# Performance work log

Hardware: AMD Instinct MI355X
Metric: run time of the kernel (lower is better)

## Reference

```python
import jax, jax.numpy as jnp
import numpy as np

DIM = 1024
HEADS = 16
HDIM = DIM // HEADS
HIDDEN = 4 * DIM
SCALE = HDIM ** -0.5


def layernorm(x, g, b, eps=1e-5):
    mu = jnp.mean(x, axis=-1, keepdims=True)
    var = jnp.var(x, axis=-1, keepdims=True)
    return (x - mu) * jax.lax.rsqrt(var + eps) * g + b


def setup_inputs() -> dict:
    key = jax.random.key(0)
    ks = jax.random.split(key, 8)
    s = 0.02
    return {
        "x": jax.random.normal(ks[0], (4, 1024, DIM), dtype=jnp.float32),
        "ln1_g": jnp.ones((DIM,), jnp.float32),
        "ln1_b": jnp.zeros((DIM,), jnp.float32),
        "ln2_g": jnp.ones((DIM,), jnp.float32),
        "ln2_b": jnp.zeros((DIM,), jnp.float32),
        "qkv_w": jax.random.normal(ks[1], (DIM, 3 * DIM), jnp.float32) * s,
        "qkv_b": jnp.zeros((3 * DIM,), jnp.float32),
        "proj_w": jax.random.normal(ks[2], (DIM, DIM), jnp.float32) * s,
        "proj_b": jnp.zeros((DIM,), jnp.float32),
        "fc1_w": jax.random.normal(ks[3], (DIM, HIDDEN), jnp.float32) * s,
        "fc1_b": jnp.zeros((HIDDEN,), jnp.float32),
        "fc2_w": jax.random.normal(ks[4], (HIDDEN, DIM), jnp.float32) * s,
        "fc2_b": jnp.zeros((DIM,), jnp.float32),
    }


def reference(x, ln1_g, ln1_b, ln2_g, ln2_b, qkv_w, qkv_b, proj_w, proj_b,
              fc1_w, fc1_b, fc2_w, fc2_b):
    B, N, C = x.shape
    # --- attention branch ---
    h = layernorm(x, ln1_g, ln1_b)
    qkv = h @ qkv_w + qkv_b                       # [B,N,3C]
    qkv = qkv.reshape(B, N, 3, HEADS, HDIM)
    q, k, v = jnp.moveaxis(qkv, 2, 0)             # each [B,N,H,Dh]
    q = jnp.swapaxes(q, 1, 2)                      # [B,H,N,Dh]
    k = jnp.swapaxes(k, 1, 2)
    v = jnp.swapaxes(v, 1, 2)
    attn = jnp.einsum('bhqd,bhkd->bhqk', q, k) * SCALE
    attn = jax.nn.softmax(attn, axis=-1)
    o = jnp.einsum('bhqk,bhkd->bhqd', attn, v)     # [B,H,N,Dh]
    o = jnp.swapaxes(o, 1, 2).reshape(B, N, C)
    x = x + (o @ proj_w + proj_b)
    # --- MLP branch ---
    h = layernorm(x, ln2_g, ln2_b)
    h = jax.nn.gelu(h @ fc1_w + fc1_b, approximate=False)
    x = x + (h @ fc2_w + fc2_b)
    return x
```

## Files before the change

kernel.cpp:

```cpp
#include <hip/hip_runtime.h>
#include <math.h>

#define DIM    1024
#define HEADS  16
#define HDIM   64
#define HIDDEN 4096
#define BATCH  4
#define SEQ    1024
#define ROWS   (BATCH * SEQ)

typedef short s16x8 __attribute__((ext_vector_type(8)));
typedef float f32x4 __attribute__((ext_vector_type(4)));

__device__ __forceinline__ float blo(unsigned int u) {
    union { unsigned int i; float f; } x; x.i = u << 16; return x.f;
}
__device__ __forceinline__ float bhi(unsigned int u) {
    union { unsigned int i; float f; } x; x.i = u & 0xffff0000u; return x.f;
}
__device__ __forceinline__ unsigned short f2b(float f) {
    union { float f; unsigned int i; } x; x.f = f;
    unsigned int r = x.i + 0x7fffu + ((x.i >> 16) & 1u);
    return (unsigned short)(r >> 16);
}

__device__ __forceinline__ float gelu_f(float x) {
    float z  = fabsf(x) * 0.70710678118f;
    float t  = __builtin_amdgcn_rcpf(__builtin_fmaf(0.3275911f, z, 1.0f));
    float p  = ((((1.061405429f * t - 1.453152027f) * t + 1.421413741f) * t
                 - 0.284496736f) * t + 0.254829592f) * t;
    float e  = exp2f(-0.72134752f * x * x);
    float w  = 0.5f * p * e;
    float phi = (x >= 0.0f) ? (1.0f - w) : w;
    return x * phi;
}

__device__ __forceinline__ size_t tidx(int row, int k, int Kdim) {
    return ((size_t)(row >> 4) * (Kdim >> 5) + (k >> 5)) * 512
         + (size_t)(((k & 31) >> 3) * 128 + (row & 15) * 8 + (k & 7));
}

__device__ __forceinline__ void gload_lds16(const void* g, void* l) {
    __builtin_amdgcn_global_load_lds(
        (const __attribute__((address_space(1))) unsigned int*)g,
        (__attribute__((address_space(3))) unsigned int*)l, 16, 0, 0);
}

__global__ __launch_bounds__(256) void prep_kernel(const float* __restrict__ x,
                                                   const float* __restrict__ g,
                                                   const float* __restrict__ b,
                                                   unsigned short* __restrict__ lnout,
                                                   const float* __restrict__ qkv_w,
                                                   unsigned short* __restrict__ wT_qkv,
                                                   const float* __restrict__ proj_w,
                                                   unsigned short* __restrict__ wT_proj,
                                                   const float* __restrict__ fc1_w,
                                                   unsigned short* __restrict__ wT_fc1,
                                                   const float* __restrict__ fc2_w,
                                                   unsigned short* __restrict__ wT_fc2) {
    __shared__ float red1[256], red2[256];
    __shared__ unsigned short T[64][68];
    const int bid = blockIdx.x;
    const int t = threadIdx.x;

    if (bid < ROWS) {
        int row = bid;
        const float* xr = x + (size_t)row * DIM;
        float4 v = *((const float4*)(xr + t * 4));
        float s  = v.x + v.y + v.z + v.w;
        float ss = v.x * v.x + v.y * v.y + v.z * v.z + v.w * v.w;
        red1[t] = s; red2[t] = ss;
        __syncthreads();
        for (int off = 128; off > 0; off >>= 1) {
            if (t < off) { red1[t] += red1[t + off]; red2[t] += red2[t + off]; }
            __syncthreads();
        }
        float mu   = red1[0] * (1.0f / DIM);
        float var  = red2[0] * (1.0f / DIM) - mu * mu;
        float rstd = rsqrtf(var + 1e-5f);
        float4 gv = *((const float4*)(g + t * 4));
        float4 bv = *((const float4*)(b + t * 4));
        ushort4 o;
        o.x = f2b((v.x - mu) * rstd * gv.x + bv.x);
        o.y = f2b((v.y - mu) * rstd * gv.y + bv.y);
        o.z = f2b((v.z - mu) * rstd * gv.z + bv.z);
        o.w = f2b((v.w - mu) * rstd * gv.w + bv.w);
        *((ushort4*)(lnout + tidx(row, t * 4, DIM))) = o;
    } else {
        int tt = bid - ROWS;
        const float* W; unsigned short* Wt; int K, N, bx, by;
        if (tt < 768) {
            W = qkv_w; Wt = wT_qkv; K = DIM; N = 3 * DIM; bx = tt % 48; by = tt / 48;
        } else if (tt < 768 + 256) {
            tt -= 768;
            W = proj_w; Wt = wT_proj; K = DIM; N = DIM; bx = tt % 16; by = tt / 16;
        } else if (tt < 768 + 256 + 1024) {
            tt -= 768 + 256;
            W = fc1_w; Wt = wT_fc1; K = DIM; N = HIDDEN; bx = tt % 64; by = tt / 64;
        } else {
            tt -= 768 + 256 + 1024;
            W = fc2_w; Wt = wT_fc2; K = HIDDEN; N = DIM; bx = tt % 16; by = tt / 16;
        }
        int n0 = bx * 64, k0 = by * 64;
        int cr = t >> 4;
        int cc = (t & 15) * 4;
        #pragma unroll
        for (int r = 0; r < 4; ++r) {
            int kk = cr + 16 * r;
            float4 v = *((const float4*)(W + (size_t)(k0 + kk) * N + n0 + cc));
            T[cc + 0][kk] = f2b(v.x);
            T[cc + 1][kk] = f2b(v.y);
            T[cc + 2][kk] = f2b(v.z);
            T[cc + 3][kk] = f2b(v.w);
        }
        __syncthreads();
        {
            int nn = t >> 2;
            int kg = (t & 3) * 16;
            #pragma unroll
            for (int p = 0; p < 2; ++p) {
                int k8 = kg + p * 8;
                ushort4 lo = *((ushort4*)&T[nn][k8]);
                ushort4 hi = *((ushort4*)&T[nn][k8 + 4]);
                unsigned short* dst = Wt + tidx(n0 + nn, k0 + k8, K);
                *((ushort4*)dst)       = lo;
                *((ushort4*)(dst + 4)) = hi;
            }
        }
    }
}

__global__ __launch_bounds__(256) void reduce_ln(const unsigned short* __restrict__ p0,
                                                 const unsigned short* __restrict__ p1,
                                                 const float* __restrict__ x,
                                                 const float* __restrict__ bias,
                                                 const float* __restrict__ g,
                                                 const float* __restrict__ b,
                                                 float* __restrict__ xout,
                                                 unsigned short* __restrict__ lnout) {
    int row = blockIdx.x;
    int t = threadIdx.x;
    size_t i = (size_t)row * DIM + t * 4;
    float4 xv = *((const float4*)(x + i));
    float4 bi = *((const float4*)(bias + t * 4));
    uint2 w0 = *((const uint2*)(p0 + i));
    uint2 w1 = *((const uint2*)(p1 + i));
    float4 v;
    v.x = xv.x + bi.x + blo(w0.x) + blo(w1.x);
    v.y = xv.y + bi.y + bhi(w0.x) + bhi(w1.x);
    v.z = xv.z + bi.z + blo(w0.y) + blo(w1.y);
    v.w = xv.w + bi.w + bhi(w0.y) + bhi(w1.y);
    *((float4*)(xout + i)) = v;

    float s  = v.x + v.y + v.z + v.w;
    float ss = v.x * v.x + v.y * v.y + v.z * v.z + v.w * v.w;
    __shared__ float red1[256], red2[256];
    red1[t] = s; red2[t] = ss;
    __syncthreads();
    for (int off = 128; off > 0; off >>= 1) {
        if (t < off) { red1[t] += red1[t + off]; red2[t] += red2[t + off]; }
        __syncthreads();
    }
    float mu   = red1[0] * (1.0f / DIM);
    float var  = red2[0] * (1.0f / DIM) - mu * mu;
    float rstd = rsqrtf(var + 1e-5f);
    float4 gv = *((const float4*)(g + t * 4));
    float4 bv = *((const float4*)(b + t * 4));
    ushort4 o;
    o.x = f2b((v.x - mu) * rstd * gv.x + bv.x);
    o.y = f2b((v.y - mu) * rstd * gv.y + bv.y);
    o.z = f2b((v.z - mu) * rstd * gv.z + bv.z);
    o.w = f2b((v.w - mu) * rstd * gv.w + bv.w);
    *((ushort4*)(lnout + tidx(row, t * 4, DIM))) = o;
}

__global__ __launch_bounds__(256, 4) void mfma_gemm(const unsigned short* __restrict__ A,
                                                 const unsigned short* __restrict__ Bt,
                                                 const float* __restrict__ bias,
                                                 void* __restrict__ Cout,
                                                 unsigned short* __restrict__ vt,
                                                 unsigned short* __restrict__ p0,
                                                 unsigned short* __restrict__ p1,
                                                 unsigned short* __restrict__ p2,
                                                 unsigned short* __restrict__ p3,
                                                 int M, int N, int K, int Ksplit, int fuse) {
    __shared__ __align__(16) short Asm[8192];
    __shared__ __align__(16) short Bsm[8192];

    const int tid  = threadIdx.x;
    const int lane = tid & 63;
    const int wave = tid >> 6;
    const int wy = wave >> 1, wx = wave & 1;
    const int lr = lane & 15;
    const int lq = lane >> 4;

    int m_t, n_t;
    {
        const int mt = gridDim.x, ntl = gridDim.y, G = 8;
        if (ntl > G) {
            int lin = blockIdx.y * mt + blockIdx.x;
            int gsz = mt * G;
            int grp = lin / gsz;
            int rem = lin - grp * gsz;
            m_t = rem % mt;
            n_t = grp * G + rem / mt;
        } else { m_t = blockIdx.x; n_t = blockIdx.y; }
    }
    const int m0 = m_t * 128, n0 = n_t * 128;
    const int kbase = blockIdx.z * Ksplit;
    const int kch = K >> 5;

    f32x4 acc[4][4];
    #pragma unroll
    for (int i = 0; i < 4; ++i)
        #pragma unroll
        for (int j = 0; j < 4; ++j)
            acc[i][j] = (f32x4){0.f, 0.f, 0.f, 0.f};

    const unsigned short* ag[4]; const unsigned short* bg[4];
    short* al[4]; short* bl[4];
    #pragma unroll
    for (int j = 0; j < 4; ++j) {
        int cid = wave * 4 + j;
        int mb  = cid >> 1;
        int kc  = cid & 1;
        ag[j] = A  + ((size_t)((m0 >> 4) + mb) * kch + (kbase >> 5) + kc) * 512 + lane * 8;
        bg[j] = Bt + ((size_t)((n0 >> 4) + mb) * kch + (kbase >> 5) + kc) * 512 + lane * 8;
        al[j] = &Asm[cid * 512];
        bl[j] = &Bsm[cid * 512];
    }

    for (int k0 = 0; k0 < Ksplit; k0 += 64) {
        #pragma unroll
        for (int j = 0; j < 4; ++j) {
            gload_lds16(ag[j], al[j]);
            gload_lds16(bg[j], bl[j]);
            ag[j] += 1024; bg[j] += 1024;
        }
        __syncthreads();
        #pragma unroll
        for (int kc = 0; kc < 2; ++kc) {
            s16x8 af[4], bf[4];
            #pragma unroll
            for (int i = 0; i < 4; ++i)
                af[i] = *((const s16x8*)&Asm[((wy * 4 + i) * 2 + kc) * 512 + lane * 8]);
            #pragma unroll
            for (int j = 0; j < 4; ++j)
                bf[j] = *((const s16x8*)&Bsm[((wx * 4 + j) * 2 + kc) * 512 + lane * 8]);
            #pragma unroll
            for (int i = 0; i < 4; ++i)
                #pragma unroll
                for (int j = 0; j < 4; ++j)
                    acc[i][j] = __builtin_amdgcn_mfma_f32_16x16x32_bf16(af[i], bf[j], acc[i][j], 0, 0, 0);
        }
        __syncthreads();
    }

    short* Wl = (wave < 2 ? Asm : Bsm) + (wave & 1) * 4096;

    if (fuse == 0 && vt && (n0 + wx * 64) >= 2 * DIM) {
        #pragma unroll
        for (int j = 0; j < 4; ++j) {
            int col = n0 + wx * 64 + j * 16 + lr;
            float bi = bias[col];
            #pragma unroll
            for (int i = 0; i < 4; ++i) {
                int row0 = m0 + wy * 64 + i * 16 + lq * 4;
                #pragma unroll
                for (int r = 0; r < 4; ++r) {
                    float val = acc[i][j][r] + bi;
                    int row = row0 + r;
                    int b_ = row >> 10, tok = row & 1023;
                    int hd = col - 2 * DIM, h_ = hd >> 6, d = hd & 63;
                    size_t o = (size_t)(b_ * 16 + h_) * 65536
                             + ((size_t)(d >> 4) * 32 + (tok >> 5)) * 512
                             + ((tok & 31) >> 3) * 128 + (d & 15) * 8 + (tok & 7);
                    vt[o] = f2b(val);
                }
            }
        }
    } else if (fuse == 3) {
        #pragma unroll
        for (int j = 0; j < 4; ++j) {
            #pragma unroll
            for (int i = 0; i < 4; ++i) {
                #pragma unroll
                for (int r = 0; r < 4; ++r) {
                    int rowL = i * 16 + lq * 4 + r;
                    int colL = (j * 16 + lr) ^ ((rowL & 7) << 3);
                    Wl[rowL * 64 + colL] = (short)f2b(acc[i][j][r]);
                }
            }
        }
        int z = blockIdx.z;
        unsigned short* P = (z == 0) ? p0 : (z == 1) ? p1 : (z == 2) ? p2 : p3;
        unsigned short* Prow = P + (size_t)(m0 + wy * 64 + lane) * N + n0 + wx * 64;
        #pragma unroll
        for (int c = 0; c < 8; ++c) {
            int colr = (c * 8) ^ ((lane & 7) << 3);
            s16x8 v = *((const s16x8*)&Wl[lane * 64 + colr]);
            *((s16x8*)&Prow[c * 8]) = v;
        }
    } else {
        #pragma unroll
        for (int j = 0; j < 4; ++j) {
            float bi = bias[n0 + wx * 64 + j * 16 + lr];
            #pragma unroll
            for (int i = 0; i < 4; ++i) {
                #pragma unroll
                for (int r = 0; r < 4; ++r) {
                    float val = acc[i][j][r] + bi;
                    if (fuse == 1) val = gelu_f(val);
                    int colL = (j & 1) * 16 + lr;
                    int hi = colL >> 3;
                    int pos = hi * 128 + (lq * 4 + r) * 8 + (lr & 7);
                    pos ^= ((pos >> 7) & 3) << 3;
                    Wl[(i * 2 + (j >> 1)) * 512 + pos] = (short)f2b(val);
                }
            }
        }
        const size_t rc0 = (size_t)((m0 + wy * 64) >> 4);
        const size_t cc0 = (size_t)((n0 + wx * 64) >> 5);
        const size_t nch = (size_t)(N >> 5);
        #pragma unroll
        for (int c = 0; c < 8; ++c) {
            int raddr = lane * 8;
            raddr ^= ((raddr >> 7) & 3) << 3;
            s16x8 v = *((const s16x8*)&Wl[c * 512 + raddr]);
            size_t chunk = (rc0 + (c >> 1)) * nch + cc0 + (c & 1);
            *((s16x8*)&((unsigned short*)Cout)[chunk * 512 + lane * 8]) = v;
        }
    }
}

__global__ __launch_bounds__(256) void reduce_kernel(const unsigned short* __restrict__ p0,
                                                     const unsigned short* __restrict__ p1,
                                                     const unsigned short* __restrict__ p2,
                                                     const unsigned short* __restrict__ p3,
                                                     int S,
                                                     const float* __restrict__ x,
                                                     const float* __restrict__ bias,
                                                     float* __restrict__ out) {
    int i = (blockIdx.x * 256 + threadIdx.x) * 8;
    int col = i & (DIM - 1);
    float4 b0 = *((const float4*)(bias + col));
    float4 b1 = *((const float4*)(bias + col + 4));
    float4 x0 = *((const float4*)(x + i));
    float4 x1 = *((const float4*)(x + i + 4));
    float a[8] = {x0.x + b0.x, x0.y + b0.y, x0.z + b0.z, x0.w + b0.w,
                  x1.x + b1.x, x1.y + b1.y, x1.z + b1.z, x1.w + b1.w};
    const unsigned short* ps[4] = {p0, p1, p2, p3};
    for (int s = 0; s < S; ++s) {
        uint4 w = *((const uint4*)(ps[s] + i));
        a[0] += blo(w.x); a[1] += bhi(w.x);
        a[2] += blo(w.y); a[3] += bhi(w.y);
        a[4] += blo(w.z); a[5] += bhi(w.z);
        a[6] += blo(w.w); a[7] += bhi(w.w);
    }
    *((float4*)(out + i))     = make_float4(a[0], a[1], a[2], a[3]);
    *((float4*)(out + i + 4)) = make_float4(a[4], a[5], a[6], a[7]);
}

__global__ __launch_bounds__(256) void fattn_mfma(const unsigned short* __restrict__ qkv,
                                                  const unsigned short* __restrict__ Vt,
                                                  unsigned short* __restrict__ out) {
    __shared__ __align__(16) short Qs[4096];
    __shared__ __align__(16) short Ks[4096];
    __shared__ __align__(16) short Vs[4096];
    __shared__ __align__(16) short Ps[64 * 72];
    __shared__ __align__(16) short OnesB[512];

    const int tid = threadIdx.x, lane = tid & 63, wave = tid >> 6;
    const int lr = lane & 15, lq = lane >> 4;
    const int L = blockIdx.x;
    const int idx = L >> 3;
    const int qt = idx & 15;
    const int bh = (L & 7) + 8 * (idx >> 4);
    const int b = bh >> 4, h = bh & 15;
    const int q0 = qt * 64;

    {
        s16x8 z = (s16x8){0,0,0,0,0,0,0,0};
        if (lr == 0) { z[0] = (short)0x3F80; z[1] = (short)0x3F80;
                       z[2] = (short)0x3F80; z[3] = (short)0x3F80;
                       z[4] = (short)0x3F80; z[5] = (short)0x3F80;
                       z[6] = (short)0x3F80; z[7] = (short)0x3F80; }
        if (wave == 0) *((s16x8*)&OnesB[lane * 8]) = z;
    }

    #pragma unroll
    for (int j = 0; j < 2; ++j) {
        int cid = wave * 2 + j;
        const unsigned short* g = qkv + ((size_t)(((b * SEQ + q0) >> 4) + (cid >> 1)) * 96
                                         + 2 * h + (cid & 1)) * 512 + lane * 8;
        gload_lds16(g, &Qs[cid * 512]);
    }

    const unsigned short* kg_[2]; const unsigned short* vg_[2];
    short *kl_[2], *vl_[2];
    #pragma unroll
    for (int j = 0; j < 2; ++j) {
        int cid = wave * 2 + j;
        kg_[j] = qkv + ((size_t)(((b * SEQ) >> 4) + (cid >> 1)) * 96
                        + 32 + 2 * h + (cid & 1)) * 512 + lane * 8;
        vg_[j] = Vt + (size_t)bh * 65536
                 + ((size_t)(cid >> 1) * 32 + (cid & 1)) * 512 + lane * 8;
        kl_[j] = &Ks[cid * 512];
        vl_[j] = &Vs[cid * 512];
    }

    f32x4 osum[5];
    #pragma unroll
    for (int d = 0; d < 5; ++d)
        osum[d] = (f32x4){0.f, 0.f, 0.f, 0.f};

    const float c = 0.125f * 1.44269504f;

    for (int k0 = 0; k0 < SEQ; k0 += 64) {
        #pragma unroll
        for (int j = 0; j < 2; ++j) {
            gload_lds16(kg_[j], kl_[j]);
            gload_lds16(vg_[j], vl_[j]);
            kg_[j] += 4 * 96 * 512;
            vg_[j] += 1024;
        }
        __syncthreads();

        f32x4 s[4];
        #pragma unroll
        for (int jb = 0; jb < 4; ++jb)
            s[jb] = (f32x4){0.f, 0.f, 0.f, 0.f};
        __builtin_amdgcn_s_setprio(1);
        #pragma unroll
        for (int kc = 0; kc < 2; ++kc) {
            s16x8 aq = *((const s16x8*)&Qs[(wave * 2 + kc) * 512 + lane * 8]);
            #pragma unroll
            for (int jb = 0; jb < 4; ++jb) {
                s16x8 bk = *((const s16x8*)&Ks[(jb * 2 + kc) * 512 + lane * 8]);
                s[jb] = __builtin_amdgcn_mfma_f32_16x16x32_bf16(aq, bk, s[jb], 0, 0, 0);
            }
        }
        __builtin_amdgcn_s_setprio(0);

        #pragma unroll
        for (int r = 0; r < 4; ++r) {
            int prow = wave * 16 + lq * 4 + r;
            #pragma unroll
            for (int jb = 0; jb < 4; ++jb)
                Ps[prow * 72 + jb * 16 + lr] = (short)f2b(exp2f(s[jb][r] * c));
        }

        __builtin_amdgcn_s_setprio(1);
        #pragma unroll
        for (int kc = 0; kc < 2; ++kc) {
            s16x8 ap = *((const s16x8*)&Ps[(wave * 16 + lr) * 72 + kc * 32 + lq * 8]);
            #pragma unroll
            for (int db = 0; db < 4; ++db) {
                s16x8 bv = *((const s16x8*)&Vs[(db * 2 + kc) * 512 + lane * 8]);
                osum[db] = __builtin_amdgcn_mfma_f32_16x16x32_bf16(ap, bv, osum[db], 0, 0, 0);
            }
            s16x8 bo = *((const s16x8*)&OnesB[lane * 8]);
            osum[4] = __builtin_amdgcn_mfma_f32_16x16x32_bf16(ap, bo, osum[4], 0, 0, 0);
        }
        __builtin_amdgcn_s_setprio(0);
        __syncthreads();
    }

    {
        int qrow = q0 + wave * 16 + lq * 4;
        #pragma unroll
        for (int r = 0; r < 4; ++r) {
            float lsum = __shfl(osum[4][r], lane & 48, 64);
            float inv = 1.0f / lsum;
            int row = b * SEQ + qrow + r;
            #pragma unroll
            for (int db = 0; db < 4; ++db)
                out[tidx(row, h * 64 + db * 16 + lr, DIM)] = f2b(osum[db][r] * inv);
        }
    }
}

extern "C" void kernel_launch(void* const* d_in, const int* in_sizes, int n_in,
                              void* d_out, int out_size, void* d_ws, size_t ws_size,
                              hipStream_t stream) {
    const float* x      = (const float*)d_in[0];
    const float* ln1_g  = (const float*)d_in[1];
    const float* ln1_b  = (const float*)d_in[2];
    const float* ln2_g  = (const float*)d_in[3];
    const float* ln2_b  = (const float*)d_in[4];
    const float* qkv_w  = (const float*)d_in[5];
    const float* qkv_b  = (const float*)d_in[6];
    const float* proj_w = (const float*)d_in[7];
    const float* proj_b = (const float*)d_in[8];
    const float* fc1_w  = (const float*)d_in[9];
    const float* fc1_b  = (const float*)d_in[10];
    const float* fc2_w  = (const float*)d_in[11];
    const float* fc2_b  = (const float*)d_in[12];
    float* out = (float*)d_out;

    char* ws = (char*)d_ws;
    unsigned short* wT_fc2  = (unsigned short*)(ws);
    unsigned short* wT_qkv  = (unsigned short*)(ws + (8u  << 20));
    unsigned short* wT_proj = (unsigned short*)(ws + (14u << 20));
    unsigned short* qkvbuf  = (unsigned short*)(ws + (16u << 20));
    unsigned short* Vt      = (unsigned short*)(ws + (40u << 20));
    unsigned short* attnout = (unsigned short*)(ws + (48u << 20));
    unsigned short* lnout   = (unsigned short*)(ws + (56u << 20));
    unsigned short* wT_fc1  = (unsigned short*)(ws + (64u << 20));
    unsigned short* gelu    = (unsigned short*)(ws + (16u << 20));
    unsigned short* pp0 = (unsigned short*)(ws + (16u << 20));
    unsigned short* pp1 = (unsigned short*)(ws + (24u << 20));
    unsigned short* fp0 = (unsigned short*)(ws + (48u << 20));
    unsigned short* fp1 = (unsigned short*)(ws + (56u << 20));
    unsigned short* fp2 = (unsigned short*)(ws + (64u << 20));
    unsigned short* fp3 = (unsigned short*)(ws + (8u  << 20));

    prep_kernel<<<ROWS + 3072, 256, 0, stream>>>(
        x, ln1_g, ln1_b, lnout,
        qkv_w, wT_qkv, proj_w, wT_proj, fc1_w, wT_fc1, fc2_w, wT_fc2);
    mfma_gemm<<<dim3(ROWS / 128, 3 * DIM / 128, 1), 256, 0, stream>>>(
        lnout, wT_qkv, qkv_b, qkvbuf, Vt, nullptr, nullptr, nullptr, nullptr,
        ROWS, 3 * DIM, DIM, DIM, 0);
    fattn_mfma<<<(SEQ / 64) * BATCH * HEADS, 256, 0, stream>>>(qkvbuf, Vt, attnout);
    mfma_gemm<<<dim3(ROWS / 128, DIM / 128, 2), 256, 0, stream>>>(
        attnout, wT_proj, proj_b, nullptr, nullptr, pp0, pp1, nullptr, nullptr,
        ROWS, DIM, DIM, DIM / 2, 3);
    reduce_ln<<<ROWS, 256, 0, stream>>>(pp0, pp1, x, proj_b, ln2_g, ln2_b, out, lnout);
    mfma_gemm<<<dim3(ROWS / 128, HIDDEN / 128, 1), 256, 0, stream>>>(
        lnout, wT_fc1, fc1_b, gelu, nullptr, nullptr, nullptr, nullptr, nullptr,
        ROWS, HIDDEN, DIM, DIM, 1);
    mfma_gemm<<<dim3(ROWS / 128, DIM / 128, 4), 256, 0, stream>>>(
        gelu, wT_fc2, fc2_b, nullptr, nullptr, fp0, fp1, fp2, fp3,
        ROWS, DIM, HIDDEN, HIDDEN / 4, 3);
    reduce_kernel<<<ROWS * DIM / 2048, 256, 0, stream>>>(
        fp0, fp1, fp2, fp3, 4, out, fc2_b, out);
}
```

Before: 319.3 us.

## Double-buffer GEMM LDS tiles to overlap global loads with MFMA

The GEMM main loop now splits shared memory into two 32-wide K buffers. It prefetches the next chunk into one buffer while computing on the other, instead of loading a full 64-wide tile and then computing. This aims to hide global-to-LDS latency behind MFMA work and to cut the number of barriers per K step. Total LDS use is unchanged, but sync ordering is subtler, and the final iteration's prefetch guard depends on Ksplit being a multiple of 64.

After: 337.4 us. +5.7%, slower.

```diff
diff --git a/kernel.cpp b/kernel.cpp
--- a/kernel.cpp
+++ b/kernel.cpp
@@ -184,8 +184,8 @@
                                                  unsigned short* __restrict__ p2,
                                                  unsigned short* __restrict__ p3,
                                                  int M, int N, int K, int Ksplit, int fuse) {
-    __shared__ __align__(16) short Asm[8192];
-    __shared__ __align__(16) short Bsm[8192];
+    __shared__ __align__(16) short Asm[2][4096];
+    __shared__ __align__(16) short Bsm[2][4096];
 
     const int tid  = threadIdx.x;
     const int lane = tid & 63;
@@ -217,46 +217,45 @@
         for (int j = 0; j < 4; ++j)
             acc[i][j] = (f32x4){0.f, 0.f, 0.f, 0.f};
 
-    const unsigned short* ag[4]; const unsigned short* bg[4];
-    short* al[4]; short* bl[4];
+    const unsigned short* ag[2]; const unsigned short* bg[2];
     #pragma unroll
-    for (int j = 0; j < 4; ++j) {
-        int cid = wave * 4 + j;
-        int mb  = cid >> 1;
-        int kc  = cid & 1;
-        ag[j] = A  + ((size_t)((m0 >> 4) + mb) * kch + (kbase >> 5) + kc) * 512 + lane * 8;
-        bg[j] = Bt + ((size_t)((n0 >> 4) + mb) * kch + (kbase >> 5) + kc) * 512 + lane * 8;
-        al[j] = &Asm[cid * 512];
-        bl[j] = &Bsm[cid * 512];
-    }
-
+    for (int j = 0; j < 2; ++j) {
+        int rc = wave * 2 + j;
+        ag[j] = A  + ((size_t)((m0 >> 4) + rc) * kch + (kbase >> 5)) * 512 + lane * 8;
+        bg[j] = Bt + ((size_t)((n0 >> 4) + rc) * kch + (kbase >> 5)) * 512 + lane * 8;
+    }
+
+#define STAGE(buf) { \
+    _Pragma("unroll") for (int j_ = 0; j_ < 2; ++j_) { \
+        gload_lds16(ag[j_], &Asm[buf][(wave * 2 + j_) * 512]); \
+        gload_lds16(bg[j_], &Bsm[buf][(wave * 2 + j_) * 512]); \
+        ag[j_] += 512; bg[j_] += 512; \
+    } }
+#define COMPUTE(buf) { \
+    s16x8 af[4], bf[4]; \
+    _Pragma("unroll") for (int i_ = 0; i_ < 4; ++i_) \
+        af[i_] = *((const s16x8*)&Asm[buf][(wy * 4 + i_) * 512 + lane * 8]); \
+    _Pragma("unroll") for (int j_ = 0; j_ < 4; ++j_) \
+        bf[j_] = *((const s16x8*)&Bsm[buf][(wx * 4 + j_) * 512 + lane * 8]); \
+    _Pragma("unroll") for (int i_ = 0; i_ < 4; ++i_) \
+        _Pragma("unroll") for (int j_ = 0; j_ < 4; ++j_) \
+            acc[i_][j_] = __builtin_amdgcn_mfma_f32_16x16x32_bf16(af[i_], bf[j_], acc[i_][j_], 0, 0, 0); \
+    }
+
+    STAGE(0);
+    __syncthreads();
     for (int k0 = 0; k0 < Ksplit; k0 += 64) {
-        #pragma unroll
-        for (int j = 0; j < 4; ++j) {
-            gload_lds16(ag[j], al[j]);
-            gload_lds16(bg[j], bl[j]);
-            ag[j] += 1024; bg[j] += 1024;
-        }
-        __syncthreads();
-        #pragma unroll
-        for (int kc = 0; kc < 2; ++kc) {
-            s16x8 af[4], bf[4];
-            #pragma unroll
-            for (int i = 0; i < 4; ++i)
-                af[i] = *((const s16x8*)&Asm[((wy * 4 + i) * 2 + kc) * 512 + lane * 8]);
-            #pragma unroll
-            for (int j = 0; j < 4; ++j)
-                bf[j] = *((const s16x8*)&Bsm[((wx * 4 + j) * 2 + kc) * 512 + lane * 8]);
-            #pragma unroll
-            for (int i = 0; i < 4; ++i)
-                #pragma unroll
-                for (int j = 0; j < 4; ++j)
-                    acc[i][j] = __builtin_amdgcn_mfma_f32_16x16x32_bf16(af[i], bf[j], acc[i][j], 0, 0, 0);
-        }
-        __syncthreads();
-    }
-
-    short* Wl = (wave < 2 ? Asm : Bsm) + (wave & 1) * 4096;
+        STAGE(1);
+        COMPUTE(0);
+        __syncthreads();
+        if (k0 + 64 < Ksplit) STAGE(0);
+        COMPUTE(1);
+        __syncthreads();
+    }
+#undef STAGE
+#undef COMPUTE
+
+    short* Wl = (wave < 2 ? (short*)Asm : (short*)Bsm) + (wave & 1) * 4096;
 
     if (fuse == 0 && vt && (n0 + wx * 64) >= 2 * DIM) {
         #pragma unroll
```
